# Kernel optimization log

Hardware: AMD Instinct MI355X
Metric: run time of the kernel (lower is better)

Reference implementation:

```python
import jax, jax.numpy as jnp
import numpy as np

EMBED_DIM = 1024
NUM_HEADS = 16
HEAD_DIM = EMBED_DIM // NUM_HEADS
L = 1024  # target/source seq len
N = 2     # batch
EPS = 1e-6


def setup_inputs() -> dict:
    key = jax.random.key(0)
    ks = jax.random.split(key, 11)
    s = 0.02
    return {
        "query": jax.random.normal(ks[0], (L, N, EMBED_DIM), jnp.float32),
        "key": jax.random.normal(ks[1], (L, N, EMBED_DIM), jnp.float32),
        "value": jax.random.normal(ks[2], (L, N, EMBED_DIM), jnp.float32),
        "Wq": jax.random.normal(ks[3], (EMBED_DIM, EMBED_DIM), jnp.float32) * s,
        "bq": jnp.zeros((EMBED_DIM,), jnp.float32),
        "Wk": jax.random.normal(ks[4], (EMBED_DIM, EMBED_DIM), jnp.float32) * s,
        "bk": jnp.zeros((EMBED_DIM,), jnp.float32),
        "Wv": jax.random.normal(ks[5], (EMBED_DIM, EMBED_DIM), jnp.float32) * s,
        "bv": jnp.zeros((EMBED_DIM,), jnp.float32),
        "Wo": jax.random.normal(ks[6], (EMBED_DIM, EMBED_DIM), jnp.float32) * s,
        "bo": jnp.zeros((EMBED_DIM,), jnp.float32),
    }


def _feature_map(x):
    # phi(x) = elu(x) + 1 (Katharopoulos et al., 2020)
    return jax.nn.elu(x) + 1.0


def reference(query, key, value, Wq, bq, Wk, bk, Wv, bv, Wo, bo):
    tgt_len, bsz, embed_dim = query.shape
    H, d = NUM_HEADS, HEAD_DIM
    # projections (torch Linear: x @ W.T + b)
    q = query @ Wq.T + bq
    k = key @ Wk.T + bk
    v = value @ Wv.T + bv
    # (L, N, E) -> (N*H, L, d)
    def to_heads(x):
        return x.reshape(-1, bsz * H, d).transpose(1, 0, 2)
    q, k, v = to_heads(q), to_heads(k), to_heads(v)
    q = _feature_map(q)
    k = _feature_map(k)
    # causal linear attention: S_t = cumsum_s<=t k_s v_s^T ; z_t = cumsum k_s
    kv = jnp.cumsum(jnp.einsum('bld,ble->blde', k, v), axis=1)  # (B*H, L, d, d)
    num = jnp.einsum('bld,blde->ble', q, kv)                    # (B*H, L, d)
    z = jnp.cumsum(k, axis=1)                                   # (B*H, L, d)
    denom = jnp.einsum('bld,bld->bl', q, z) + EPS               # (B*H, L)
    attn = num / denom[..., None]
    # (N*H, L, d) -> (L, N, E)
    attn = attn.transpose(1, 0, 2).reshape(tgt_len, bsz, embed_dim)
    return attn @ Wo.T + bo
```

## Files before the change

### kernel.cpp

```cpp
#include <hip/hip_runtime.h>
#include <cmath>


#define EPS 1e-6f

typedef short bf16x8 __attribute__((ext_vector_type(8)));
typedef float f32x4 __attribute__((ext_vector_type(4)));

__device__ __forceinline__ float b2f(ushort u) {
    union { unsigned u32; float f; } x; x.u32 = ((unsigned)u) << 16; return x.f;
}
__device__ __forceinline__ ushort f2b(float f) {
    union { float f; unsigned u; } x; x.f = f;
    unsigned r = (x.u + 0x7fffu + ((x.u >> 16) & 1u)) >> 16;
    return (ushort)r;
}
__device__ __forceinline__ void gload16(const void* g, void* l) {
    __builtin_amdgcn_global_load_lds(
        (__attribute__((address_space(1))) void*)(uintptr_t)g,
        (__attribute__((address_space(3))) void*)l,
        16, 0, 0);
}

template<int KSTEPS>
__device__ __forceinline__ void gemm_mainloop7(const ushort* __restrict__ A,
                                               const ushort* __restrict__ B,
                                               int brow, int bcol, int kbeg,
                                               ushort* Sh, f32x4 acc[4][4]) {
    const int K = 1024;
    const int BUFE = 16384;
    int tid = threadIdx.x;
    int w = tid >> 6, lane = tid & 63;
    int fr = lane & 15, hi = lane >> 4;
    int khalf = w >> 2, quad = w & 3;
    int wr = quad >> 1, wc = quad & 1;

    const ushort* gsrc[4];
    int ldst[4];
    #pragma unroll
    for (int i = 0; i < 4; i++) {
        int s = (w * 4 + i) * 64 + lane;
        const ushort* base; int r, sl;
        if (s < 1024) { r = s >> 3; sl = s & 7; base = A + (size_t)(brow + r) * K; }
        else { int s2 = s - 1024; r = s2 >> 3; sl = s2 & 7; base = B + (size_t)(bcol + r) * K; }
        int orig = sl ^ (r & 7);
        int khw = orig >> 2, c16 = orig & 3;
        gsrc[i] = base + kbeg + khw * (KSTEPS * 32) + c16 * 8;
        ldst[i] = (w * 4 + i) * 512;
    }

    int ea[4], eb[4];
    #pragma unroll
    for (int m = 0; m < 4; m++) {
        int ra = wr * 64 + m * 16 + fr;
        ea[m] = ra * 64 + (((khalf * 4 + hi) ^ (ra & 7)) * 8);
    }
    #pragma unroll
    for (int n = 0; n < 4; n++) {
        int rb = wc * 64 + n * 16 + fr;
        eb[n] = 8192 + rb * 64 + (((khalf * 4 + hi) ^ (rb & 7)) * 8);
    }

    #pragma unroll
    for (int m = 0; m < 4; m++)
        #pragma unroll
        for (int n = 0; n < 4; n++)
            acc[m][n] = (f32x4){0.f, 0.f, 0.f, 0.f};

    #pragma unroll
    for (int i = 0; i < 4; i++) gload16(gsrc[i], Sh + ldst[i]);
    __syncthreads();

    for (int t = 0; t < KSTEPS; ++t) {
        if (t + 1 < KSTEPS) {
            ushort* Sn = Sh + ((t + 1) & 1) * BUFE;
            #pragma unroll
            for (int i = 0; i < 4; i++) gload16(gsrc[i] + (t + 1) * 32, Sn + ldst[i]);
        }
        const ushort* Bc = Sh + (t & 1) * BUFE;
        bf16x8 af[4], bf[4];
        #pragma unroll
        for (int m = 0; m < 4; m++) af[m] = *(const bf16x8*)&Bc[ea[m]];
        #pragma unroll
        for (int n = 0; n < 4; n++) bf[n] = *(const bf16x8*)&Bc[eb[n]];
        #pragma unroll
        for (int m = 0; m < 4; m++)
            #pragma unroll
            for (int n = 0; n < 4; n++)
                acc[m][n] = __builtin_amdgcn_mfma_f32_16x16x32_bf16(af[m], bf[n], acc[m][n], 0, 0, 0);
        __syncthreads();
    }

    float* red = (float*)Sh;
    if (khalf == 1) {
        #pragma unroll
        for (int m = 0; m < 4; m++)
            #pragma unroll
            for (int n = 0; n < 4; n++)
                *(f32x4*)&red[(quad * 16 + m * 4 + n) * 256 + lane * 4] = acc[m][n];
    }
    __syncthreads();
    if (khalf == 0) {
        #pragma unroll
        for (int m = 0; m < 4; m++)
            #pragma unroll
            for (int n = 0; n < 4; n++)
                acc[m][n] += *(const f32x4*)&red[(quad * 16 + m * 4 + n) * 256 + lane * 4];
    }
}

__global__ __launch_bounds__(512) void gemm_proj(
    const ushort* __restrict__ Aq, const ushort* __restrict__ Ak, const ushort* __restrict__ Av,
    const ushort* __restrict__ Bq, const ushort* __restrict__ Bk, const ushort* __restrict__ Bv,
    const float* __restrict__ bq, const float* __restrict__ bk, const float* __restrict__ bv,
    ushort* __restrict__ oq, ushort* __restrict__ ok, ushort* __restrict__ ov) {
    __shared__ ushort Sh[2 * 16384];
    int bid = blockIdx.x;
    int swz = (bid & 7) * 48 + (bid >> 3);
    int z = swz >> 7;
    int rem = swz & 127;
    int brow = (rem >> 3) * 128, bcol = (rem & 7) * 128;
    const ushort* A = (z == 0) ? Aq : (z == 1) ? Ak : Av;
    const ushort* B = (z == 0) ? Bq : (z == 1) ? Bk : Bv;
    const float* bias = (z == 0) ? bq : (z == 1) ? bk : bv;
    f32x4 acc[4][4];
    gemm_mainloop7<16>(A, B, brow, bcol, 0, Sh, acc);
    int tid = threadIdx.x, w = tid >> 6, lane = tid & 63;
    if (w >= 4) return;
    int fr = lane & 15, hi = lane >> 4;
    int wr = (w >> 1) & 1, wc = w & 1;
    #pragma unroll
    for (int m = 0; m < 4; m++)
        #pragma unroll
        for (int n = 0; n < 4; n++)
            #pragma unroll
            for (int r = 0; r < 4; r++) {
                int grow = brow + wr * 64 + m * 16 + hi * 4 + r;
                int gcol = bcol + wc * 64 + n * 16 + fr;
                float v = acc[m][n][r] + bias[gcol];
                int l = grow >> 1, nb2 = grow & 1, h = gcol >> 6, dd = gcol & 63;
                if (z == 2) {
                    ov[(size_t)((nb2 * 16 + h) * 64 + dd) * 1024 + l] = f2b(v);
                } else {
                    v = (v > 0.f) ? v + 1.f : __expf(v);
                    ushort* out = (z == 0) ? oq : ok;
                    out[(size_t)((nb2 * 16 + h) * 1024 + l) * 64 + dd] = f2b(v);
                }
            }
}

__global__ __launch_bounds__(512) void gemm_outk(const ushort* __restrict__ A,
                                                 const ushort* __restrict__ B,
                                                 float* __restrict__ pbuf) {
    __shared__ ushort Sh[2 * 16384];
    int bid = blockIdx.x;
    int swz = (bid & 7) * 32 + (bid >> 3);
    int z = swz >> 7;
    int rem = swz & 127;
    int brow = (rem >> 3) * 128, bcol = (rem & 7) * 128;
    f32x4 acc[4][4];
    gemm_mainloop7<8>(A, B, brow, bcol, z * 512, Sh, acc);
    int tid = threadIdx.x, w = tid >> 6, lane = tid & 63;
    if (w >= 4) return;
    int fr = lane & 15, hi = lane >> 4;
    int wr = (w >> 1) & 1, wc = w & 1;
    float* out = pbuf + (size_t)z * 2097152;
    #pragma unroll
    for (int m = 0; m < 4; m++)
        #pragma unroll
        for (int n = 0; n < 4; n++)
            #pragma unroll
            for (int r = 0; r < 4; r++) {
                int grow = brow + wr * 64 + m * 16 + hi * 4 + r;
                int gcol = bcol + wc * 64 + n * 16 + fr;
                out[(size_t)grow * 1024 + gcol] = acc[m][n][r];
            }
}

__global__ __launch_bounds__(256) void reduce_out(const float* __restrict__ p,
                                                  const float* __restrict__ bias,
                                                  float* __restrict__ out) {
    int i = blockIdx.x * 256 + threadIdx.x;
    float4 a = ((const float4*)p)[i];
    float4 b = ((const float4*)(p + 2097152))[i];
    float4 bb = ((const float4*)bias)[i & 255];
    float4 o;
    o.x = a.x + b.x + bb.x;
    o.y = a.y + b.y + bb.y;
    o.z = a.z + b.z + bb.z;
    o.w = a.w + b.w + bb.w;
    ((float4*)out)[i] = o;
}

__global__ __launch_bounds__(256) void cast_all(
    const float* __restrict__ i0, const float* __restrict__ i1, const float* __restrict__ i2,
    const float* __restrict__ i3, const float* __restrict__ i4, const float* __restrict__ i5,
    const float* __restrict__ i6,
    ushort* __restrict__ o0, ushort* __restrict__ o1, ushort* __restrict__ o2,
    ushort* __restrict__ o3, ushort* __restrict__ o4, ushort* __restrict__ o5,
    ushort* __restrict__ o6) {
    int z = blockIdx.z;
    const float* in = (z == 0) ? i0 : (z == 1) ? i1 : (z == 2) ? i2 :
                      (z == 3) ? i3 : (z == 4) ? i4 : (z == 5) ? i5 : i6;
    ushort* out = (z == 0) ? o0 : (z == 1) ? o1 : (z == 2) ? o2 :
                  (z == 3) ? o3 : (z == 4) ? o4 : (z == 5) ? o5 : o6;
    int n4 = (z < 3) ? 524288 : 262144;
    int i = blockIdx.x * 256 + threadIdx.x;
    if (i < n4) {
        float4 f = ((const float4*)in)[i];
        ushort4 o; o.x = f2b(f.x); o.y = f2b(f.y); o.z = f2b(f.z); o.w = f2b(f.w);
        ((ushort4*)out)[i] = o;
    }
}

__global__ __launch_bounds__(256) void chunk_sums(const ushort* __restrict__ kh,
                                                  const ushort* __restrict__ vt,
                                                  float* __restrict__ St,
                                                  float* __restrict__ zc) {
    int c = blockIdx.x, b = blockIdx.y, tid = threadIdx.x;
    __shared__ float Kl[64][64];
    __shared__ float Vl[64][65];
    const ushort* Kg = kh + (size_t)(b * 1024 + c * 64) * 64;
    for (int i = tid; i < 1024; i += 256) {
        ushort4 k4 = ((const ushort4*)Kg)[i];
        ((float4*)Kl)[i] = make_float4(b2f(k4.x), b2f(k4.y), b2f(k4.z), b2f(k4.w));
        int e = i >> 4, s4 = (i & 15) << 2;
        ushort4 v4 = *(const ushort4*)&vt[(size_t)(b * 64 + e) * 1024 + c * 64 + s4];
        Vl[e][s4 + 0] = b2f(v4.x); Vl[e][s4 + 1] = b2f(v4.y);
        Vl[e][s4 + 2] = b2f(v4.z); Vl[e][s4 + 3] = b2f(v4.w);
    }
    __syncthreads();
    int e = tid & 63, d0 = (tid >> 6) * 16;
    float s[16] = {};
    for (int ss = 0; ss < 64; ss++) {
        float ve = Vl[e][ss];
        #pragma unroll
        for (int i = 0; i < 16; i++) s[i] += Kl[ss][d0 + i] * ve;
    }
    float* So = St + (size_t)(b * 16 + c) * 4096 + e * 64 + d0;
    #pragma unroll
    for (int k = 0; k < 4; k++)
        *(float4*)&So[k * 4] = make_float4(s[4*k], s[4*k+1], s[4*k+2], s[4*k+3]);
    if (tid < 64) {
        float z = 0.f;
        for (int ss = 0; ss < 64; ss++) z += Kl[ss][tid];
        zc[(size_t)(b * 16 + c) * 64 + tid] = z;
    }
}

__global__ __launch_bounds__(256) void prefix_chunks(const float* __restrict__ St,
                                                     ushort* __restrict__ Spt,
                                                     float* __restrict__ zc) {
    int b = blockIdx.x, by = blockIdx.y, tid = threadIdx.x;
    int e = by * 16 + (tid >> 4);
    int d0 = (tid & 15) * 4;
    size_t base = (size_t)b * 65536 + (size_t)e * 64 + d0;
    float run[4] = {};
    for (int c = 0; c < 16; c++) {
        float4 v = *(const float4*)&St[base + (size_t)c * 4096];
        ushort4 o;
        o.x = f2b(run[0]); o.y = f2b(run[1]); o.z = f2b(run[2]); o.w = f2b(run[3]);
        *(ushort4*)&Spt[base + (size_t)c * 4096] = o;
        run[0] += v.x; run[1] += v.y; run[2] += v.z; run[3] += v.w;
    }
    if (by == 0 && tid < 64) {
        float rz = 0.f;
        for (int c = 0; c < 16; c++) {
            size_t idx = ((size_t)b * 16 + c) * 64 + tid;
            float t = zc[idx];
            zc[idx] = rz;
            rz += t;
        }
    }
}

__global__ __launch_bounds__(256) void attn_chunk(const ushort* __restrict__ qh,
                                                  const ushort* __restrict__ kh,
                                                  const ushort* __restrict__ vt,
                                                  const ushort* __restrict__ Spt,
                                                  const float* __restrict__ zc,
                                                  ushort* __restrict__ attn) {
    int c = blockIdx.x, b = blockIdx.y, tid = threadIdx.x;
    int w = tid >> 6, lane = tid & 63;
    int fr = lane & 15, hi = lane >> 4;
    __shared__ ushort Q[4096], Kt[4096], VT[4096], SP[4096], P[4096];
    __shared__ float den[64];

    {
        const ushort* bases[4];
        bases[0] = qh + (size_t)(b * 1024 + c * 64) * 64;
        bases[1] = kh + (size_t)(b * 1024 + c * 64) * 64;
        bases[2] = vt;
        bases[3] = Spt + (size_t)(b * 16 + c) * 4096;
        ushort* dsts[4] = {Q, Kt, VT, SP};
        #pragma unroll
        for (int tl = 0; tl < 4; tl++) {
            #pragma unroll
            for (int j = 0; j < 2; j++) {
                int i = w * 64 + lane + 256 * j;
                int row = i >> 3, sl = i & 7;
                int col = (sl ^ (row & 7)) * 8;
                const ushort* src;
                if (tl == 2) src = vt + (size_t)(b * 64 + row) * 1024 + c * 64 + col;
                else         src = bases[tl] + (size_t)row * 64 + col;
                gload16(src, dsts[tl] + w * 512 + 2048 * j);
            }
        }
    }
    __syncthreads();

    int frow = w * 16 + fr;
    int fkey = fr & 7;
    bf16x8 aq[2];
    #pragma unroll
    for (int kk = 0; kk < 2; kk++)
        aq[kk] = *(const bf16x8*)&Q[frow * 64 + ((kk * 4 + hi) ^ fkey) * 8];
    f32x4 pc[4];
    #pragma unroll
    for (int n = 0; n < 4; n++) {
        pc[n] = (f32x4){0.f, 0.f, 0.f, 0.f};
        #pragma unroll
        for (int kk = 0; kk < 2; kk++) {
            bf16x8 bk_ = *(const bf16x8*)&Kt[(n * 16 + fr) * 64 + ((kk * 4 + hi) ^ fkey) * 8];
            pc[n] = __builtin_amdgcn_mfma_f32_16x16x32_bf16(aq[kk], bk_, pc[n], 0, 0, 0);
        }
    }
    float denp[4] = {0.f, 0.f, 0.f, 0.f};
    #pragma unroll
    for (int n = 0; n < 4; n++)
        #pragma unroll
        for (int r = 0; r < 4; r++) {
            int t = w * 16 + hi * 4 + r;
            int s = n * 16 + fr;
            float v = (s <= t) ? pc[n][r] : 0.f;
            denp[r] += v;
            P[t * 64 + (((s >> 3) ^ (t & 7)) * 8) + (s & 7)] = f2b(v);
        }
    #pragma unroll
    for (int r = 0; r < 4; r++) {
        denp[r] += __shfl_xor(denp[r], 1);
        denp[r] += __shfl_xor(denp[r], 2);
        denp[r] += __shfl_xor(denp[r], 4);
        denp[r] += __shfl_xor(denp[r], 8);
    }
    if (fr == 0) {
        #pragma unroll
        for (int r = 0; r < 4; r++) den[w * 16 + hi * 4 + r] = denp[r];
    }
    __syncthreads();

    if (tid < 64) {
        int t = tid;
        const float* zg = zc + (size_t)(b * 16 + c) * 64;
        float a = 0.f;
        for (int d = 0; d < 64; d++)
            a += b2f(Q[t * 64 + (((d >> 3) ^ (t & 7)) * 8) + (d & 7)]) * zg[d];
        den[t] += a;
    }

    bf16x8 ap[2];
    #pragma unroll
    for (int kk = 0; kk < 2; kk++)
        ap[kk] = *(const bf16x8*)&P[frow * 64 + ((kk * 4 + hi) ^ fkey) * 8];
    f32x4 nacc[4];
    #pragma unroll
    for (int n = 0; n < 4; n++) {
        nacc[n] = (f32x4){0.f, 0.f, 0.f, 0.f};
        #pragma unroll
        for (int kk = 0; kk < 2; kk++) {
            bf16x8 bs = *(const bf16x8*)&SP[(n * 16 + fr) * 64 + ((kk * 4 + hi) ^ fkey) * 8];
            nacc[n] = __builtin_amdgcn_mfma_f32_16x16x32_bf16(aq[kk], bs, nacc[n], 0, 0, 0);
        }
        #pragma unroll
        for (int kk = 0; kk < 2; kk++) {
            bf16x8 bv = *(const bf16x8*)&VT[(n * 16 + fr) * 64 + ((kk * 4 + hi) ^ fkey) * 8];
            nacc[n] = __builtin_amdgcn_mfma_f32_16x16x32_bf16(ap[kk], bv, nacc[n], 0, 0, 0);
        }
    }
    __syncthreads();

    int nb = b >> 4, h = b & 15;
    #pragma unroll
    for (int n = 0; n < 4; n++)
        #pragma unroll
        for (int r = 0; r < 4; r++) {
            int t = w * 16 + hi * 4 + r;
            int e = n * 16 + fr;
            int l = c * 64 + t;
            float val = nacc[n][r] / (den[t] + EPS);
            attn[(size_t)(l * 2 + nb) * 1024 + h * 64 + e] = f2b(val);
        }
}

extern "C" void kernel_launch(void* const* d_in, const int* in_sizes, int n_in,
                              void* d_out, int out_size, void* d_ws, size_t ws_size,
                              hipStream_t stream) {
    const float* query = (const float*)d_in[0];
    const float* key_  = (const float*)d_in[1];
    const float* value = (const float*)d_in[2];
    const float* Wq = (const float*)d_in[3];
    const float* bq = (const float*)d_in[4];
    const float* Wk = (const float*)d_in[5];
    const float* bk = (const float*)d_in[6];
    const float* Wv = (const float*)d_in[7];
    const float* bv = (const float*)d_in[8];
    const float* Wo = (const float*)d_in[9];
    const float* bo = (const float*)d_in[10];

    ushort* qbuf = (ushort*)d_ws;
    ushort* kbuf = qbuf + 2097152;
    ushort* vbuf = kbuf + 2097152;
    ushort* wqb  = vbuf + 2097152;
    ushort* wkb  = wqb + 1048576;
    ushort* wvb  = wkb + 1048576;
    ushort* wob  = wvb + 1048576;
    ushort* qh   = wob + 1048576;
    ushort* kh   = qh + 2097152;
    ushort* vt   = kh + 2097152;
    float*  St   = (float*)(vt + 2097152);
    ushort* Spt  = (ushort*)(St + 2097152);
    float*  zc   = (float*)(Spt + 2097152);
    float*  pbuf = zc + 32768;
    ushort* attn = qbuf;

    cast_all<<<dim3(2048, 1, 7), 256, 0, stream>>>(query, key_, value, Wq, Wk, Wv, Wo,
                                                   qbuf, kbuf, vbuf, wqb, wkb, wvb, wob);

    gemm_proj<<<384, 512, 0, stream>>>(qbuf, kbuf, vbuf, wqb, wkb, wvb,
                                       bq, bk, bv, qh, kh, vt);

    chunk_sums<<<dim3(16, 32), 256, 0, stream>>>(kh, vt, St, zc);
    prefix_chunks<<<dim3(32, 4), 256, 0, stream>>>(St, Spt, zc);
    attn_chunk<<<dim3(16, 32), 256, 0, stream>>>(qh, kh, vt, Spt, zc, attn);

    gemm_outk<<<256, 512, 0, stream>>>(attn, wob, pbuf);
    reduce_out<<<2048, 256, 0, stream>>>(pbuf, bo, (float*)d_out);
}
```

Before: 85.60 us.

## Replace intra-block split-K with grid-level split-K and bf16 partial buffers

The GEMM mainloop drops its 512-thread intra-block K-split and LDS reduction. Each kernel now uses 256-thread blocks, each owning a 128x128 tile over a smaller K range. The projection GEMM is split 2-way in K across blocks (768 blocks), stores bf16 partials, and gains a separate combine kernel that applies bias, the feature map and the head-layout scatter. The output GEMM is split 4-way with bf16 partials reduced in reduce_out. The goal is more blocks and occupancy and less LDS traffic, at the cost of an extra launch, extra global round-trips, and precision loss from rounding the partial sums to bf16.

After: 91.79 us. +7.2%, slower.

```diff
diff --git a/kernel.cpp b/kernel.cpp
--- a/kernel.cpp
+++ b/kernel.cpp
@@ -23,29 +23,26 @@
 }
 
 template<int KSTEPS>
-__device__ __forceinline__ void gemm_mainloop7(const ushort* __restrict__ A,
+__device__ __forceinline__ void gemm_mainloop8(const ushort* __restrict__ A,
                                                const ushort* __restrict__ B,
                                                int brow, int bcol, int kbeg,
                                                ushort* Sh, f32x4 acc[4][4]) {
     const int K = 1024;
-    const int BUFE = 16384;
+    const int BUFE = 8192;
     int tid = threadIdx.x;
     int w = tid >> 6, lane = tid & 63;
     int fr = lane & 15, hi = lane >> 4;
-    int khalf = w >> 2, quad = w & 3;
-    int wr = quad >> 1, wc = quad & 1;
+    int wr = w >> 1, wc = w & 1;
 
     const ushort* gsrc[4];
     int ldst[4];
     #pragma unroll
     for (int i = 0; i < 4; i++) {
         int s = (w * 4 + i) * 64 + lane;
-        const ushort* base; int r, sl;
-        if (s < 1024) { r = s >> 3; sl = s & 7; base = A + (size_t)(brow + r) * K; }
-        else { int s2 = s - 1024; r = s2 >> 3; sl = s2 & 7; base = B + (size_t)(bcol + r) * K; }
-        int orig = sl ^ (r & 7);
-        int khw = orig >> 2, c16 = orig & 3;
-        gsrc[i] = base + kbeg + khw * (KSTEPS * 32) + c16 * 8;
+        const ushort* base; int r, c;
+        if (s < 512) { r = s >> 2; c = s & 3; base = A + (size_t)(brow + r) * K; }
+        else { int s2 = s - 512; r = s2 >> 2; c = s2 & 3; base = B + (size_t)(bcol + r) * K; }
+        gsrc[i] = base + kbeg + ((c ^ ((r >> 1) & 3)) * 8);
         ldst[i] = (w * 4 + i) * 512;
     }
 
@@ -53,12 +50,12 @@
     #pragma unroll
     for (int m = 0; m < 4; m++) {
         int ra = wr * 64 + m * 16 + fr;
-        ea[m] = ra * 64 + (((khalf * 4 + hi) ^ (ra & 7)) * 8);
+        ea[m] = ra * 32 + ((hi ^ ((ra >> 1) & 3)) * 8);
     }
     #pragma unroll
     for (int n = 0; n < 4; n++) {
         int rb = wc * 64 + n * 16 + fr;
-        eb[n] = 8192 + rb * 64 + (((khalf * 4 + hi) ^ (rb & 7)) * 8);
+        eb[n] = 4096 + rb * 32 + ((hi ^ ((rb >> 1) & 3)) * 8);
     }
 
     #pragma unroll
@@ -90,45 +87,28 @@
                 acc[m][n] = __builtin_amdgcn_mfma_f32_16x16x32_bf16(af[m], bf[n], acc[m][n], 0, 0, 0);
         __syncthreads();
     }
-
-    float* red = (float*)Sh;
-    if (khalf == 1) {
-        #pragma unroll
-        for (int m = 0; m < 4; m++)
-            #pragma unroll
-            for (int n = 0; n < 4; n++)
-                *(f32x4*)&red[(quad * 16 + m * 4 + n) * 256 + lane * 4] = acc[m][n];
-    }
-    __syncthreads();
-    if (khalf == 0) {
-        #pragma unroll
-        for (int m = 0; m < 4; m++)
-            #pragma unroll
-            for (int n = 0; n < 4; n++)
-                acc[m][n] += *(const f32x4*)&red[(quad * 16 + m * 4 + n) * 256 + lane * 4];
-    }
-}
-
-__global__ __launch_bounds__(512) void gemm_proj(
+}
+
+__global__ __launch_bounds__(256) void gemm_proj(
     const ushort* __restrict__ Aq, const ushort* __restrict__ Ak, const ushort* __restrict__ Av,
     const ushort* __restrict__ Bq, const ushort* __restrict__ Bk, const ushort* __restrict__ Bv,
-    const float* __restrict__ bq, const float* __restrict__ bk, const float* __restrict__ bv,
-    ushort* __restrict__ oq, ushort* __restrict__ ok, ushort* __restrict__ ov) {
-    __shared__ ushort Sh[2 * 16384];
+    ushort* __restrict__ pbuf) {
+    __shared__ ushort Sh[2 * 8192];
     int bid = blockIdx.x;
-    int swz = (bid & 7) * 48 + (bid >> 3);
-    int z = swz >> 7;
-    int rem = swz & 127;
-    int brow = (rem >> 3) * 128, bcol = (rem & 7) * 128;
+    int swz = (bid & 7) * 96 + (bid >> 3);
+    int z = swz >> 8;
+    int rem = swz & 255;
+    int kh = rem >> 7;
+    int rem2 = rem & 127;
+    int brow = (rem2 >> 3) * 128, bcol = (rem2 & 7) * 128;
     const ushort* A = (z == 0) ? Aq : (z == 1) ? Ak : Av;
     const ushort* B = (z == 0) ? Bq : (z == 1) ? Bk : Bv;
-    const float* bias = (z == 0) ? bq : (z == 1) ? bk : bv;
     f32x4 acc[4][4];
-    gemm_mainloop7<16>(A, B, brow, bcol, 0, Sh, acc);
+    gemm_mainloop8<16>(A, B, brow, bcol, kh * 512, Sh, acc);
     int tid = threadIdx.x, w = tid >> 6, lane = tid & 63;
-    if (w >= 4) return;
     int fr = lane & 15, hi = lane >> 4;
-    int wr = (w >> 1) & 1, wc = w & 1;
+    int wr = w >> 1, wc = w & 1;
+    ushort* pp = pbuf + (size_t)(z * 2 + kh) * 2097152;
     #pragma unroll
     for (int m = 0; m < 4; m++)
         #pragma unroll
@@ -137,34 +117,60 @@
             for (int r = 0; r < 4; r++) {
                 int grow = brow + wr * 64 + m * 16 + hi * 4 + r;
                 int gcol = bcol + wc * 64 + n * 16 + fr;
-                float v = acc[m][n][r] + bias[gcol];
-                int l = grow >> 1, nb2 = grow & 1, h = gcol >> 6, dd = gcol & 63;
-                if (z == 2) {
-                    ov[(size_t)((nb2 * 16 + h) * 64 + dd) * 1024 + l] = f2b(v);
-                } else {
-                    v = (v > 0.f) ? v + 1.f : __expf(v);
-                    ushort* out = (z == 0) ? oq : ok;
-                    out[(size_t)((nb2 * 16 + h) * 1024 + l) * 64 + dd] = f2b(v);
-                }
+                pp[(size_t)grow * 1024 + gcol] = f2b(acc[m][n][r]);
             }
 }
 
-__global__ __launch_bounds__(512) void gemm_outk(const ushort* __restrict__ A,
+__global__ __launch_bounds__(256) void combine_proj(const ushort* __restrict__ pbuf,
+                                                    const float* __restrict__ bq,
+                                                    const float* __restrict__ bk,
+                                                    const float* __restrict__ bv,
+                                                    ushort* __restrict__ oq,
+                                                    ushort* __restrict__ ok,
+                                                    ushort* __restrict__ ov) {
+    int z = blockIdx.z;
+    int idx = blockIdx.x * 256 + threadIdx.x;
+    int row = idx >> 7, c0 = (idx & 127) * 8;
+    const float* bias = (z == 0) ? bq : (z == 1) ? bk : bv;
+    const ushort* p0 = pbuf + (size_t)(z * 2) * 2097152 + (size_t)row * 1024 + c0;
+    bf16x8 a = *(const bf16x8*)p0;
+    bf16x8 b = *(const bf16x8*)(p0 + 2097152);
+    int l = row >> 1, nb = row & 1, h = c0 >> 6, dd0 = c0 & 63;
+    float v[8];
+    #pragma unroll
+    for (int j = 0; j < 8; j++)
+        v[j] = b2f((ushort)a[j]) + b2f((ushort)b[j]) + bias[c0 + j];
+    if (z < 2) {
+        bf16x8 o;
+        #pragma unroll
+        for (int j = 0; j < 8; j++) {
+            float t = (v[j] > 0.f) ? v[j] + 1.f : __expf(v[j]);
+            o[j] = (short)f2b(t);
+        }
+        ushort* out = (z == 0) ? oq : ok;
+        *(bf16x8*)&out[(size_t)((nb * 16 + h) * 1024 + l) * 64 + dd0] = o;
+    } else {
+        #pragma unroll
+        for (int j = 0; j < 8; j++)
+            ov[(size_t)((nb * 16 + h) * 64 + dd0 + j) * 1024 + l] = f2b(v[j]);
+    }
+}
+
+__global__ __launch_bounds__(256) void gemm_outk(const ushort* __restrict__ A,
                                                  const ushort* __restrict__ B,
-                                                 float* __restrict__ pbuf) {
-    __shared__ ushort Sh[2 * 16384];
+                                                 ushort* __restrict__ pbuf) {
+    __shared__ ushort Sh[2 * 8192];
     int bid = blockIdx.x;
-    int swz = (bid & 7) * 32 + (bid >> 3);
+    int swz = (bid & 7) * 64 + (bid >> 3);
     int z = swz >> 7;
     int rem = swz & 127;
     int brow = (rem >> 3) * 128, bcol = (rem & 7) * 128;
     f32x4 acc[4][4];
-    gemm_mainloop7<8>(A, B, brow, bcol, z * 512, Sh, acc);
+    gemm_mainloop8<8>(A, B, brow, bcol, z * 256, Sh, acc);
     int tid = threadIdx.x, w = tid >> 6, lane = tid & 63;
-    if (w >= 4) return;
     int fr = lane & 15, hi = lane >> 4;
-    int wr = (w >> 1) & 1, wc = w & 1;
-    float* out = pbuf + (size_t)z * 2097152;
+    int wr = w >> 1, wc = w & 1;
+    ushort* pp = pbuf + (size_t)z * 2097152;
     #pragma unroll
     for (int m = 0; m < 4; m++)
         #pragma unroll
@@ -173,23 +179,25 @@
             for (int r = 0; r < 4; r++) {
                 int grow = brow + wr * 64 + m * 16 + hi * 4 + r;
                 int gcol = bcol + wc * 64 + n * 16 + fr;
-                out[(size_t)grow * 1024 + gcol] = acc[m][n][r];
+                pp[(size_t)grow * 1024 + gcol] = f2b(acc[m][n][r]);
             }
 }
 
-__global__ __launch_bounds__(256) void reduce_out(const float* __restrict__ p,
+__global__ __launch_bounds__(256) void reduce_out(const ushort* __restrict__ pbuf,
                                                   const float* __restrict__ bias,
                                                   float* __restrict__ out) {
-    int i = blockIdx.x * 256 + threadIdx.x;
-    float4 a = ((const float4*)p)[i];
-    float4 b = ((const float4*)(p + 2097152))[i];
-    float4 bb = ((const float4*)bias)[i & 255];
-    float4 o;
-    o.x = a.x + b.x + bb.x;
-    o.y = a.y + b.y + bb.y;
-    o.z = a.z + b.z + bb.z;
-    o.w = a.w + b.w + bb.w;
-    ((float4*)out)[i] = o;
+    int idx = blockIdx.x * 256 + threadIdx.x;
+    int row = idx >> 7, c0 = (idx & 127) * 8;
+    const ushort* p = pbuf + (size_t)row * 1024 + c0;
+    bf16x8 a = *(const bf16x8*)p;
+    bf16x8 b = *(const bf16x8*)(p + 2097152);
+    bf16x8 c = *(const bf16x8*)(p + 4194304);
+    bf16x8 d = *(const bf16x8*)(p + 6291456);
+    float* o = out + (size_t)row * 1024 + c0;
+    #pragma unroll
+    for (int j = 0; j < 8; j++)
+        o[j] = b2f((ushort)a[j]) + b2f((ushort)b[j]) + b2f((ushort)c[j]) +
+               b2f((ushort)d[j]) + bias[c0 + j];
 }
 
 __global__ __launch_bounds__(256) void cast_all(
@@ -420,19 +428,19 @@
     float*  St   = (float*)(vt + 2097152);
     ushort* Spt  = (ushort*)(St + 2097152);
     float*  zc   = (float*)(Spt + 2097152);
-    float*  pbuf = zc + 32768;
+    ushort* pbuf = (ushort*)(zc + 32768);
     ushort* attn = qbuf;
 
     cast_all<<<dim3(2048, 1, 7), 256, 0, stream>>>(query, key_, value, Wq, Wk, Wv, Wo,
                                                    qbuf, kbuf, vbuf, wqb, wkb, wvb, wob);
 
-    gemm_proj<<<384, 512, 0, stream>>>(qbuf, kbuf, vbuf, wqb, wkb, wvb,
-                                       bq, bk, bv, qh, kh, vt);
+    gemm_proj<<<768, 256, 0, stream>>>(qbuf, kbuf, vbuf, wqb, wkb, wvb, pbuf);
+    combine_proj<<<dim3(1024, 1, 3), 256, 0, stream>>>(pbuf, bq, bk, bv, qh, kh, vt);
 
     chunk_sums<<<dim3(16, 32), 256, 0, stream>>>(kh, vt, St, zc);
     prefix_chunks<<<dim3(32, 4), 256, 0, stream>>>(St, Spt, zc);
     attn_chunk<<<dim3(16, 32), 256, 0, stream>>>(qh, kh, vt, Spt, zc, attn);
 
-    gemm_outk<<<256, 512, 0, stream>>>(attn, wob, pbuf);
-    reduce_out<<<2048, 256, 0, stream>>>(pbuf, bo, (float*)d_out);
-}
+    gemm_outk<<<512, 256, 0, stream>>>(attn, wob, pbuf);
+    reduce_out<<<1024, 256, 0, stream>>>(pbuf, bo, (float*)d_out);
+}
```

## Replace split-K-within-block GEMM with 4-stage pipelined 256-thread mainloop

Applied to the files above, without the earlier changes.

The shared GEMM mainloop drops the 8-wave split-K-within-block scheme and its LDS reduction. It now uses 4 waves per block with a 4-buffer LDS ring and prefetches two k-steps ahead, using explicit vmcnt waits and raw barriers instead of __syncthreads. Launch bounds allow two blocks per CU, so occupancy comes from more blocks rather than more waves. This removes the final cross-wave reduction and overlaps loads more deeply, at the cost of fewer waves per block hiding latency and twice as many k iterations.

Result: faster. 81.86 us (median of 3 runs) (-4.4%).

```diff
diff --git a/kernel.cpp b/kernel.cpp
--- a/kernel.cpp
+++ b/kernel.cpp
@@ -23,29 +23,26 @@
 }
 
 template<int KSTEPS>
-__device__ __forceinline__ void gemm_mainloop7(const ushort* __restrict__ A,
+__device__ __forceinline__ void gemm_mainloop9(const ushort* __restrict__ A,
                                                const ushort* __restrict__ B,
                                                int brow, int bcol, int kbeg,
                                                ushort* Sh, f32x4 acc[4][4]) {
     const int K = 1024;
-    const int BUFE = 16384;
+    const int BUFE = 8192;
     int tid = threadIdx.x;
     int w = tid >> 6, lane = tid & 63;
     int fr = lane & 15, hi = lane >> 4;
-    int khalf = w >> 2, quad = w & 3;
-    int wr = quad >> 1, wc = quad & 1;
+    int wr = w >> 1, wc = w & 1;
 
     const ushort* gsrc[4];
     int ldst[4];
     #pragma unroll
     for (int i = 0; i < 4; i++) {
         int s = (w * 4 + i) * 64 + lane;
-        const ushort* base; int r, sl;
-        if (s < 1024) { r = s >> 3; sl = s & 7; base = A + (size_t)(brow + r) * K; }
-        else { int s2 = s - 1024; r = s2 >> 3; sl = s2 & 7; base = B + (size_t)(bcol + r) * K; }
-        int orig = sl ^ (r & 7);
-        int khw = orig >> 2, c16 = orig & 3;
-        gsrc[i] = base + kbeg + khw * (KSTEPS * 32) + c16 * 8;
+        const ushort* base; int r, c;
+        if (s < 512) { r = s >> 2; c = s & 3; base = A + (size_t)(brow + r) * K; }
+        else { int s2 = s - 512; r = s2 >> 2; c = s2 & 3; base = B + (size_t)(bcol + r) * K; }
+        gsrc[i] = base + kbeg + ((c ^ ((r >> 1) & 3)) * 8);
         ldst[i] = (w * 4 + i) * 512;
     }
 
@@ -53,12 +50,12 @@
     #pragma unroll
     for (int m = 0; m < 4; m++) {
         int ra = wr * 64 + m * 16 + fr;
-        ea[m] = ra * 64 + (((khalf * 4 + hi) ^ (ra & 7)) * 8);
+        ea[m] = ra * 32 + ((hi ^ ((ra >> 1) & 3)) * 8);
     }
     #pragma unroll
     for (int n = 0; n < 4; n++) {
         int rb = wc * 64 + n * 16 + fr;
-        eb[n] = 8192 + rb * 64 + (((khalf * 4 + hi) ^ (rb & 7)) * 8);
+        eb[n] = 4096 + rb * 32 + ((hi ^ ((rb >> 1) & 3)) * 8);
     }
 
     #pragma unroll
@@ -68,16 +65,25 @@
             acc[m][n] = (f32x4){0.f, 0.f, 0.f, 0.f};
 
     #pragma unroll
-    for (int i = 0; i < 4; i++) gload16(gsrc[i], Sh + ldst[i]);
-    __syncthreads();
+    for (int p = 0; p < 2; p++)
+        #pragma unroll
+        for (int i = 0; i < 4; i++)
+            gload16(gsrc[i] + p * 32, Sh + p * BUFE + ldst[i]);
 
     for (int t = 0; t < KSTEPS; ++t) {
-        if (t + 1 < KSTEPS) {
-            ushort* Sn = Sh + ((t + 1) & 1) * BUFE;
+        if (t + 2 < KSTEPS) {
+            ushort* Sn = Sh + ((t + 2) & 3) * BUFE;
             #pragma unroll
-            for (int i = 0; i < 4; i++) gload16(gsrc[i] + (t + 1) * 32, Sn + ldst[i]);
-        }
-        const ushort* Bc = Sh + (t & 1) * BUFE;
+            for (int i = 0; i < 4; i++) gload16(gsrc[i] + (t + 2) * 32, Sn + ldst[i]);
+            asm volatile("s_waitcnt vmcnt(8)" ::: "memory");
+        } else if (t + 1 < KSTEPS) {
+            asm volatile("s_waitcnt vmcnt(4)" ::: "memory");
+        } else {
+            asm volatile("s_waitcnt vmcnt(0)" ::: "memory");
+        }
+        __builtin_amdgcn_s_barrier();
+        __builtin_amdgcn_sched_barrier(0);
+        const ushort* Bc = Sh + (t & 3) * BUFE;
         bf16x8 af[4], bf[4];
         #pragma unroll
         for (int m = 0; m < 4; m++) af[m] = *(const bf16x8*)&Bc[ea[m]];
@@ -88,33 +94,15 @@
             #pragma unroll
             for (int n = 0; n < 4; n++)
                 acc[m][n] = __builtin_amdgcn_mfma_f32_16x16x32_bf16(af[m], bf[n], acc[m][n], 0, 0, 0);
-        __syncthreads();
-    }
-
-    float* red = (float*)Sh;
-    if (khalf == 1) {
-        #pragma unroll
-        for (int m = 0; m < 4; m++)
-            #pragma unroll
-            for (int n = 0; n < 4; n++)
-                *(f32x4*)&red[(quad * 16 + m * 4 + n) * 256 + lane * 4] = acc[m][n];
-    }
-    __syncthreads();
-    if (khalf == 0) {
-        #pragma unroll
-        for (int m = 0; m < 4; m++)
-            #pragma unroll
-            for (int n = 0; n < 4; n++)
-                acc[m][n] += *(const f32x4*)&red[(quad * 16 + m * 4 + n) * 256 + lane * 4];
-    }
-}
-
-__global__ __launch_bounds__(512) void gemm_proj(
+    }
+}
+
+__global__ __launch_bounds__(256, 2) void gemm_proj(
     const ushort* __restrict__ Aq, const ushort* __restrict__ Ak, const ushort* __restrict__ Av,
     const ushort* __restrict__ Bq, const ushort* __restrict__ Bk, const ushort* __restrict__ Bv,
     const float* __restrict__ bq, const float* __restrict__ bk, const float* __restrict__ bv,
     ushort* __restrict__ oq, ushort* __restrict__ ok, ushort* __restrict__ ov) {
-    __shared__ ushort Sh[2 * 16384];
+    __shared__ ushort Sh[4 * 8192];
     int bid = blockIdx.x;
     int swz = (bid & 7) * 48 + (bid >> 3);
     int z = swz >> 7;
@@ -124,11 +112,10 @@
     const ushort* B = (z == 0) ? Bq : (z == 1) ? Bk : Bv;
     const float* bias = (z == 0) ? bq : (z == 1) ? bk : bv;
     f32x4 acc[4][4];
-    gemm_mainloop7<16>(A, B, brow, bcol, 0, Sh, acc);
+    gemm_mainloop9<32>(A, B, brow, bcol, 0, Sh, acc);
     int tid = threadIdx.x, w = tid >> 6, lane = tid & 63;
-    if (w >= 4) return;
     int fr = lane & 15, hi = lane >> 4;
-    int wr = (w >> 1) & 1, wc = w & 1;
+    int wr = w >> 1, wc = w & 1;
     #pragma unroll
     for (int m = 0; m < 4; m++)
         #pragma unroll
@@ -149,21 +136,20 @@
             }
 }
 
-__global__ __launch_bounds__(512) void gemm_outk(const ushort* __restrict__ A,
-                                                 const ushort* __restrict__ B,
-                                                 float* __restrict__ pbuf) {
-    __shared__ ushort Sh[2 * 16384];
+__global__ __launch_bounds__(256, 2) void gemm_outk(const ushort* __restrict__ A,
+                                                    const ushort* __restrict__ B,
+                                                    float* __restrict__ pbuf) {
+    __shared__ ushort Sh[4 * 8192];
     int bid = blockIdx.x;
     int swz = (bid & 7) * 32 + (bid >> 3);
     int z = swz >> 7;
     int rem = swz & 127;
     int brow = (rem >> 3) * 128, bcol = (rem & 7) * 128;
     f32x4 acc[4][4];
-    gemm_mainloop7<8>(A, B, brow, bcol, z * 512, Sh, acc);
+    gemm_mainloop9<16>(A, B, brow, bcol, z * 512, Sh, acc);
     int tid = threadIdx.x, w = tid >> 6, lane = tid & 63;
-    if (w >= 4) return;
     int fr = lane & 15, hi = lane >> 4;
-    int wr = (w >> 1) & 1, wc = w & 1;
+    int wr = w >> 1, wc = w & 1;
     float* out = pbuf + (size_t)z * 2097152;
     #pragma unroll
     for (int m = 0; m < 4; m++)
@@ -426,13 +412,13 @@
     cast_all<<<dim3(2048, 1, 7), 256, 0, stream>>>(query, key_, value, Wq, Wk, Wv, Wo,
                                                    qbuf, kbuf, vbuf, wqb, wkb, wvb, wob);
 
-    gemm_proj<<<384, 512, 0, stream>>>(qbuf, kbuf, vbuf, wqb, wkb, wvb,
+    gemm_proj<<<384, 256, 0, stream>>>(qbuf, kbuf, vbuf, wqb, wkb, wvb,
                                        bq, bk, bv, qh, kh, vt);
 
     chunk_sums<<<dim3(16, 32), 256, 0, stream>>>(kh, vt, St, zc);
     prefix_chunks<<<dim3(32, 4), 256, 0, stream>>>(St, Spt, zc);
     attn_chunk<<<dim3(16, 32), 256, 0, stream>>>(qh, kh, vt, Spt, zc, attn);
 
-    gemm_outk<<<256, 512, 0, stream>>>(attn, wob, pbuf);
+    gemm_outk<<<256, 256, 0, stream>>>(attn, wob, pbuf);
     reduce_out<<<2048, 256, 0, stream>>>(pbuf, bo, (float*)d_out);
 }
```
